# Optimization experiments

Measured on AMD Instinct MI355X. Metric: run time of the kernel, lower is better.

Reference implementation:

```python
import jax, jax.numpy as jnp
from jax import lax
import numpy as np

B, DIM, L_IN = 8, 512, 4096
SCALE = 2
KSIZE = 17
DN = ('NCH', 'OIH', 'NCH')  # conv1d dimension numbers


def _aa_kernel(kernel_size: int, scale: int) -> np.ndarray:
    # replicates scipy.signal.kaiser_atten / kaiser_beta / windows.kaiser
    atten = 2.285 * (kernel_size - 1) * np.pi * (1.0 / scale) + 7.95
    if atten > 50:
        beta = 0.1102 * (atten - 8.7)
    elif atten > 21:
        beta = 0.5842 * (atten - 21) ** 0.4 + 0.07886 * (atten - 21)
    else:
        beta = 0.0
    win = np.kaiser(kernel_size, beta)
    xk = np.arange(kernel_size) - kernel_size // 2
    k = np.sinc(xk / scale) * win  # normalized sinc, same as torch.sinc
    return (k / k.sum()).astype(np.float32)


def setup_inputs() -> dict:
    key = jax.random.key(0)
    k1, k2, k3, k4, k5 = jax.random.split(key, 5)
    kconv = 2 * SCALE - 1
    return {
        'x': jax.random.normal(k1, (B, DIM, L_IN), dtype=jnp.float32),
        'conv_w': jax.random.normal(k2, (DIM, DIM, kconv), dtype=jnp.float32) * (1.0 / np.sqrt(DIM * kconv)),
        'conv_b': jax.random.normal(k3, (DIM,), dtype=jnp.float32) * 0.01,
        'aa_kernel': jnp.asarray(_aa_kernel(KSIZE, SCALE)),
        'proj_w': jax.random.normal(k4, (DIM, DIM), dtype=jnp.float32) * (1.0 / np.sqrt(DIM)),
        'proj_b': jax.random.normal(k5, (DIM,), dtype=jnp.float32) * 0.01,
    }


def reference(x, conv_w, conv_b, aa_kernel, proj_w, proj_b):
    s = SCALE
    # zero-insertion upsample + Conv1d(dim,dim,2s-1,pad=s-1) fused via lhs_dilation.
    # Torch zero-inserts to length l*s (trailing s-1 zeros), so right pad is 2s-2.
    y = lax.conv_general_dilated(
        x, conv_w, window_strides=(1,), padding=[(s - 1, 2 * s - 2)],
        lhs_dilation=(s,), dimension_numbers=DN,
    ) + conv_b[None, :, None]  # [B, D, l*s]
    # depthwise anti-alias filter (same Kaiser-sinc kernel per channel)
    dw = jnp.broadcast_to(aa_kernel, (DIM, 1, KSIZE))
    y = lax.conv_general_dilated(
        y, dw, window_strides=(1,), padding=[(KSIZE // 2, KSIZE // 2)],
        feature_group_count=DIM, dimension_numbers=DN,
    )
    # pointwise 1x1 projection
    return jnp.einsum('bdl,ed->bel', y, proj_w) + proj_b[None, :, None]
```

## Files before the change

kernel.cpp:

```cpp
#include <hip/hip_runtime.h>
#include <hip/hip_bf16.h>

#define BB_   8
#define DIM_  512
#define LIN_  4096
#define LOUT_ 8192

typedef __attribute__((ext_vector_type(8))) __bf16 bf16x8;
typedef __attribute__((ext_vector_type(4))) float  f32x4;
typedef __attribute__((ext_vector_type(8))) unsigned short u16x8;

__device__ __forceinline__ float bf2f(unsigned short u) {
  union { unsigned int i; float f; } x;
  x.i = ((unsigned int)u) << 16;
  return x.f;
}

__device__ __forceinline__ unsigned short f2bf(float f) {
  unsigned int u = __float_as_uint(f);
  return (unsigned short)((u + 0x7fffu + ((u >> 16) & 1u)) >> 16);
}

__device__ __forceinline__ void gload16(const void* g, void* l) {
  __builtin_amdgcn_global_load_lds(
      (__attribute__((address_space(1))) void*)(g),
      (__attribute__((address_space(3))) void*)(l), 16, 0, 0);
}

__global__ __launch_bounds__(256) void k_prep(const float* __restrict__ proj_w,
                                              const float* __restrict__ conv_w,
                                              const float* __restrict__ conv_b,
                                              const float* __restrict__ x,
                                              unsigned short* __restrict__ Mst,
                                              float* __restrict__ Pcb,
                                              unsigned short* __restrict__ Xbt) {
  __shared__ __align__(16) float sm[4160];
  const int bx  = blockIdx.x;
  const int tid = threadIdx.x;

  if (bx < 192) {
    float* Pt = sm;
    float* Wt = sm + 1088;
    const int kk = bx >> 6;
    const int t6 = bx & 63;
    const int et = (t6 >> 3) << 6;
    const int it = (t6 & 7) << 6;
    const int tx = tid & 15, ty = tid >> 4;
    const int le = tid & 63, lg = tid >> 6;
    float acc[4][4] = {};
    for (int d0 = 0; d0 < DIM_; d0 += 16) {
      {
        const float4 v = *(const float4*)&proj_w[(size_t)(et + le) * DIM_ + d0 + lg * 4];
        Pt[(lg * 4 + 0) * 68 + le] = v.x;
        Pt[(lg * 4 + 1) * 68 + le] = v.y;
        Pt[(lg * 4 + 2) * 68 + le] = v.z;
        Pt[(lg * 4 + 3) * 68 + le] = v.w;
      }
#pragma unroll
      for (int r = 0; r < 4; ++r) {
        const int dl = r * 4 + lg;
        Wt[dl * 68 + le] = conv_w[(size_t)(d0 + dl) * (DIM_ * 3) + (it + le) * 3 + kk];
      }
      __syncthreads();
#pragma unroll
      for (int dl = 0; dl < 16; ++dl) {
        const float4 pv = *(const float4*)&Pt[dl * 68 + ty * 4];
        const float4 wv = *(const float4*)&Wt[dl * 68 + tx * 4];
        const float pa[4] = {pv.x, pv.y, pv.z, pv.w};
        const float wa[4] = {wv.x, wv.y, wv.z, wv.w};
#pragma unroll
        for (int a = 0; a < 4; ++a)
#pragma unroll
          for (int b = 0; b < 4; ++b) acc[a][b] += pa[a] * wa[b];
      }
      __syncthreads();
    }
#pragma unroll
    for (int a = 0; a < 4; ++a) {
      uint2 pk;
      pk.x = (unsigned int)f2bf(acc[a][0]) | ((unsigned int)f2bf(acc[a][1]) << 16);
      pk.y = (unsigned int)f2bf(acc[a][2]) | ((unsigned int)f2bf(acc[a][3]) << 16);
      *(uint2*)&Mst[(size_t)(kk * DIM_ + et + ty * 4 + a) * DIM_ + it + tx * 4] = pk;
    }
  } else if (bx < 320) {
    const int idx = bx - 192;
    const int e = idx * 4 + (tid >> 6);
    const int j = tid & 63;
    float s = 0.f;
#pragma unroll
    for (int d = j; d < DIM_; d += 64) s += proj_w[(size_t)e * DIM_ + d] * conv_b[d];
#pragma unroll
    for (int off = 32; off > 0; off >>= 1) s += __shfl_down(s, off, 64);
    if (j == 0) Pcb[e] = s;
  } else {
    const int bc = bx - 320;
    const int bb = bc >> 9;
    const int dt = ((bc >> 6) & 7) << 6;
    const int lt = (bc & 63) << 6;
    const int lr  = tid >> 4;
    const int lc4 = (tid & 15) << 2;
#pragma unroll
    for (int r = 0; r < 4; ++r) {
      const int d = r * 16 + lr;
      const float4 v = *(const float4*)&x[((size_t)(bb * DIM_ + dt + d) << 12) + lt + lc4];
      float* row = sm + d * 65 + lc4;
      row[0] = v.x; row[1] = v.y; row[2] = v.z; row[3] = v.w;
    }
    __syncthreads();
#pragma unroll
    for (int rr = 0; rr < 2; ++rr) {
      const int flat = rr * 256 + tid;
      const int l  = flat >> 3;
      const int d8 = (flat & 7) << 3;
      unsigned int w[4];
#pragma unroll
      for (int p = 0; p < 4; ++p) {
        const float f0 = sm[(d8 + 2 * p + 0) * 65 + l];
        const float f1 = sm[(d8 + 2 * p + 1) * 65 + l];
        w[p] = (unsigned int)f2bf(f0) | ((unsigned int)f2bf(f1) << 16);
      }
      uint4 pk; pk.x = w[0]; pk.y = w[1]; pk.z = w[2]; pk.w = w[3];
      *(uint4*)&Xbt[((size_t)(bb * LIN_ + lt + l) << 9) + dt + d8] = pk;
    }
  }
}

__global__ __launch_bounds__(512, 1) void k_fused(const unsigned short* __restrict__ Xbt,
                                                  const unsigned short* __restrict__ Mst,
                                                  const float* __restrict__ Pcb,
                                                  const float* __restrict__ aa,
                                                  const float* __restrict__ proj_b,
                                                  float* __restrict__ out) {
  __shared__ __align__(16) char lds[131072];
  const int tid = threadIdx.x;
  const int bid = blockIdx.x;
  const int wgs   = (bid & 7) * 128 + (bid >> 3);
  const int ntile = wgs >> 3;
  const int etile = wgs & 7;
  const int bb = ntile >> 4;
  const int L0 = (ntile & 15) << 8;
  const int l0g = L0 - 16;
  const int e0 = etile << 6;

  const int wave = tid >> 6;
  const int lane = tid & 63;

  const unsigned short* src[4];
  int ldso[4];
  {
    const int rl = lane >> 2;
    const int sl = lane & 3;
    const int ch = sl ^ ((rl >> 1) & 3);
#pragma unroll
    for (int i = 0; i < 4; ++i) {
      const int u  = wave + 8 * i;
      const int uu = (u >= 30) ? (u - 30) : u;
      const unsigned short* p;
      if (uu < 12) {
        const int kk = uu >> 2;
        const int er = e0 + ((uu & 3) << 4) + rl;
        p = Mst + ((size_t)(kk * 512 + er) << 9);
      } else {
        int labs = l0g + (uu - 12) * 16 + rl;
        labs = labs < 0 ? 0 : (labs > 4095 ? 4095 : labs);
        p = Xbt + ((size_t)(bb * LIN_ + labs) << 9);
      }
      src[i] = p + (ch << 3);
      ldso[i] = u << 10;
    }
  }

#define STAGE_(kt_, buf_)                              \
  do {                                                 \
    char* base_ = lds + (buf_) * 32768;                \
    gload16(src[0] + (kt_) * 32, base_ + ldso[0]);     \
    gload16(src[1] + (kt_) * 32, base_ + ldso[1]);     \
    gload16(src[2] + (kt_) * 32, base_ + ldso[2]);     \
    gload16(src[3] + (kt_) * 32, base_ + ldso[3]);     \
  } while (0)

  const int wm = wave >> 1;
  const int wn = wave & 1;
  const int lrow = lane & 15;
  const int lc   = lane >> 4;
  const int asl  = lc ^ ((lrow >> 1) & 3);
  const char* A0 = lds + ((wm * 48 + lrow) * 64 + asl * 16);
  const char* B0 = lds + (12288 + (wn * 144 + lrow) * 64 + asl * 16);

  f32x4 acc[3][9] = {};
  bf16x8 afr[2][3], bfr[2][9];

  STAGE_(0, 0); STAGE_(1, 1);
  asm volatile("s_waitcnt vmcnt(4)" ::: "memory");
  __builtin_amdgcn_s_barrier();
  __builtin_amdgcn_sched_barrier(0);
#pragma unroll
  for (int mt = 0; mt < 3; ++mt) afr[0][mt] = *(const bf16x8*)(A0 + mt * 1024);
#pragma unroll
  for (int nt = 0; nt < 9; ++nt) bfr[0][nt] = *(const bf16x8*)(B0 + nt * 1024);

#pragma unroll
  for (int kt = 0; kt < 16; ++kt) {
    const int cur = kt & 1, nxt = cur ^ 1;
    if (kt < 14) {
      STAGE_(kt + 2, (kt + 2) & 3);
      asm volatile("s_waitcnt vmcnt(4)" ::: "memory");
    } else {
      asm volatile("s_waitcnt vmcnt(0)" ::: "memory");
    }
    __builtin_amdgcn_s_barrier();
    __builtin_amdgcn_sched_barrier(0);

    if (kt < 15) {
      const int bo = ((kt + 1) & 3) * 32768;
#pragma unroll
      for (int mt = 0; mt < 3; ++mt)
        afr[nxt][mt] = *(const bf16x8*)(A0 + bo + mt * 1024);
#pragma unroll
      for (int nt = 0; nt < 9; ++nt)
        bfr[nxt][nt] = *(const bf16x8*)(B0 + bo + nt * 1024);
    }

    __builtin_amdgcn_s_setprio(1);
#pragma unroll
    for (int mt = 0; mt < 3; ++mt)
#pragma unroll
      for (int nt = 0; nt < 9; ++nt)
        acc[mt][nt] = __builtin_amdgcn_mfma_f32_16x16x32_bf16(bfr[cur][nt],
                                                              afr[cur][mt],
                                                              acc[mt][nt], 0, 0, 0);
    __builtin_amdgcn_s_setprio(0);
  }
#undef STAGE_
  __builtin_amdgcn_s_barrier();

  unsigned short* Ut = (unsigned short*)lds;
#pragma unroll
  for (int mt = 0; mt < 3; ++mt) {
    const int m = wm * 48 + mt * 16 + lrow;
#pragma unroll
    for (int nt = 0; nt < 9; ++nt) {
      const int lcol = wn * 144 + nt * 16 + (lc << 2);
      uint2 pk;
      pk.x = (unsigned int)f2bf(acc[mt][nt][0]) | ((unsigned int)f2bf(acc[mt][nt][1]) << 16);
      pk.y = (unsigned int)f2bf(acc[mt][nt][2]) | ((unsigned int)f2bf(acc[mt][nt][3]) << 16);
      *(uint2*)&Ut[m * 296 + lcol] = pk;
    }
  }
  __syncthreads();

  const int el  = tid >> 3;
  const int lt0 = (tid & 7) << 5;
  const int e   = e0 + el;
  const float pcb = Pcb[e];
  const float pb  = proj_b[e];
  float sa[17];
#pragma unroll
  for (int j = 0; j < 17; ++j) sa[j] = aa[j];
  const unsigned short* u0r = Ut + (size_t)el * 296;
  const unsigned short* u1r = Ut + (size_t)(64 + el) * 296;
  const unsigned short* u2r = Ut + (size_t)(128 + el) * 296;
  const bool edge = (L0 == 0) || (L0 == 3840);
  float* orow = out + (((size_t)(bb * 512 + e)) << 13) + 2 * (size_t)(L0 + lt0);

#pragma unroll
  for (int cc = 0; cc < 4; ++cc) {
    const int c0 = lt0 + 8 * cc + 12;
    float E[17], O[16];
    if (!edge) {
      const u16x8 e0v = *(const u16x8*)(u1r + c0 - 4);
      const u16x8 e1v = *(const u16x8*)(u1r + c0 + 4);
      const u16x8 e2v = *(const u16x8*)(u1r + c0 + 12);
      const u16x8 a0v = *(const u16x8*)(u0r + c0 - 4);
      const u16x8 a1v = *(const u16x8*)(u0r + c0 + 4);
      const u16x8 a2v = *(const u16x8*)(u0r + c0 + 12);
      const u16x8 b0v = *(const u16x8*)(u2r + c0 - 4);
      const u16x8 b1v = *(const u16x8*)(u2r + c0 + 4);
      const u16x8 b2v = *(const u16x8*)(u2r + c0 + 12);
      unsigned short ue[24], ua[24], ub[24];
#pragma unroll
      for (int j = 0; j < 8; ++j) {
        ue[j] = e0v[j]; ue[j + 8] = e1v[j]; ue[j + 16] = e2v[j];
        ua[j] = a0v[j]; ua[j + 8] = a1v[j]; ua[j + 16] = a2v[j];
        ub[j] = b0v[j]; ub[j + 8] = b1v[j]; ub[j + 16] = b2v[j];
      }
#pragma unroll
      for (int j = 0; j < 17; ++j) E[j] = bf2f(ue[4 + j]) + pcb;
#pragma unroll
      for (int j = 0; j < 16; ++j) O[j] = bf2f(ua[4 + j]) + pcb + bf2f(ub[5 + j]);
    } else {
      const int lt = L0 + lt0 + 8 * cc;
#pragma unroll
      for (int j = 0; j < 17; ++j) {
        const int l = lt - 4 + j;
        E[j] = (l >= 0 && l < 4096) ? (bf2f(u1r[c0 + j]) + pcb) : 0.f;
      }
#pragma unroll
      for (int j = 0; j < 16; ++j) {
        const int l = lt - 4 + j;
        float v = 0.f;
        if (l >= 0 && l < 4096) {
          v = bf2f(u0r[c0 + j]) + pcb;
          if (l + 1 < 4096) v += bf2f(u2r[c0 + j + 1]);
        }
        O[j] = v;
      }
    }
    float res[16];
#pragma unroll
    for (int t = 0; t < 8; ++t) {
      float se = 0.f, so = 0.f;
#pragma unroll
      for (int q = 0; q <= 8; ++q) {
        se += sa[2 * q] * E[t + q];
        so += sa[2 * q] * O[t + q];
      }
#pragma unroll
      for (int q = 0; q < 8; ++q) {
        se += sa[2 * q + 1] * O[t + q];
        so += sa[2 * q + 1] * E[t + q + 1];
      }
      res[2 * t]     = se + pb;
      res[2 * t + 1] = so + pb;
    }
#pragma unroll
    for (int c2 = 0; c2 < 4; ++c2)
      *(float4*)(orow + 16 * cc + 4 * c2) = *(const float4*)&res[4 * c2];
  }
}

extern "C" void kernel_launch(void* const* d_in, const int* in_sizes, int n_in,
                              void* d_out, int out_size, void* d_ws, size_t ws_size,
                              hipStream_t stream) {
  const float* x      = (const float*)d_in[0];
  const float* conv_w = (const float*)d_in[1];
  const float* conv_b = (const float*)d_in[2];
  const float* aa     = (const float*)d_in[3];
  const float* proj_w = (const float*)d_in[4];
  const float* proj_b = (const float*)d_in[5];
  float* out = (float*)d_out;

  char* ws = (char*)d_ws;
  unsigned short* Mst = (unsigned short*)ws;
  float*          Pcb = (float*)(ws + 1572864);
  unsigned short* Xbt = (unsigned short*)(ws + 1574912);

  k_prep<<<dim3(4416, 1, 1), 256, 0, stream>>>(proj_w, conv_w, conv_b, x, Mst, Pcb, Xbt);
  k_fused<<<dim3(1024, 1, 1), 512, 0, stream>>>(Xbt, Mst, Pcb, aa, proj_b, out);
}
```

Before: 322.0 us.

## Split GEMM main loop into two interleaved phases with staged global loads

Restructures the MFMA main loop from register double-buffered fragments into two half-phases per k-step. Each phase loads part of the B fragments from LDS, issues half of the global-to-LDS prefetches, synchronizes, then runs its MFMA subset. The aim is to cut register pressure and interleave memory issue with compute, in the style of ping-pong scheduling. It adds three barriers per iteration, exposes LDS read latency with lgkmcnt(0) waits before the MFMAs, and changes the vmcnt accounting, which risks stalls or correctness issues.

```diff
diff --git a/kernel.cpp b/kernel.cpp
--- a/kernel.cpp
+++ b/kernel.cpp
@@ -170,11 +170,15 @@
     }
   }
 
-#define STAGE_(kt_, buf_)                              \
+#define STAGE2A_(kt_, buf_)                            \
   do {                                                 \
     char* base_ = lds + (buf_) * 32768;                \
     gload16(src[0] + (kt_) * 32, base_ + ldso[0]);     \
     gload16(src[1] + (kt_) * 32, base_ + ldso[1]);     \
+  } while (0)
+#define STAGE2B_(kt_, buf_)                            \
+  do {                                                 \
+    char* base_ = lds + (buf_) * 32768;                \
     gload16(src[2] + (kt_) * 32, base_ + ldso[2]);     \
     gload16(src[3] + (kt_) * 32, base_ + ldso[3]);     \
   } while (0)
@@ -188,51 +192,58 @@
   const char* B0 = lds + (12288 + (wn * 144 + lrow) * 64 + asl * 16);
 
   f32x4 acc[3][9] = {};
-  bf16x8 afr[2][3], bfr[2][9];
-
-  STAGE_(0, 0); STAGE_(1, 1);
+
+  STAGE2A_(0, 0); STAGE2B_(0, 0);
+  STAGE2A_(1, 1); STAGE2B_(1, 1);
   asm volatile("s_waitcnt vmcnt(4)" ::: "memory");
   __builtin_amdgcn_s_barrier();
-  __builtin_amdgcn_sched_barrier(0);
-#pragma unroll
-  for (int mt = 0; mt < 3; ++mt) afr[0][mt] = *(const bf16x8*)(A0 + mt * 1024);
-#pragma unroll
-  for (int nt = 0; nt < 9; ++nt) bfr[0][nt] = *(const bf16x8*)(B0 + nt * 1024);
 
 #pragma unroll
   for (int kt = 0; kt < 16; ++kt) {
-    const int cur = kt & 1, nxt = cur ^ 1;
-    if (kt < 14) {
-      STAGE_(kt + 2, (kt + 2) & 3);
-      asm volatile("s_waitcnt vmcnt(4)" ::: "memory");
-    } else {
-      asm volatile("s_waitcnt vmcnt(0)" ::: "memory");
-    }
+    const int bo = (kt & 3) * 32768;
+    bf16x8 af[3], bfv[9];
+
+#pragma unroll
+    for (int mt = 0; mt < 3; ++mt) af[mt] = *(const bf16x8*)(A0 + bo + mt * 1024);
+#pragma unroll
+    for (int nt = 0; nt < 4; ++nt) bfv[nt] = *(const bf16x8*)(B0 + bo + nt * 1024);
+    if (kt < 14) STAGE2A_(kt + 2, (kt + 2) & 3);
     __builtin_amdgcn_s_barrier();
+    asm volatile("s_waitcnt lgkmcnt(0)" ::: "memory");
     __builtin_amdgcn_sched_barrier(0);
-
-    if (kt < 15) {
-      const int bo = ((kt + 1) & 3) * 32768;
-#pragma unroll
-      for (int mt = 0; mt < 3; ++mt)
-        afr[nxt][mt] = *(const bf16x8*)(A0 + bo + mt * 1024);
-#pragma unroll
-      for (int nt = 0; nt < 9; ++nt)
-        bfr[nxt][nt] = *(const bf16x8*)(B0 + bo + nt * 1024);
-    }
-
     __builtin_amdgcn_s_setprio(1);
 #pragma unroll
     for (int mt = 0; mt < 3; ++mt)
 #pragma unroll
-      for (int nt = 0; nt < 9; ++nt)
-        acc[mt][nt] = __builtin_amdgcn_mfma_f32_16x16x32_bf16(bfr[cur][nt],
-                                                              afr[cur][mt],
+      for (int nt = 0; nt < 4; ++nt)
+        acc[mt][nt] = __builtin_amdgcn_mfma_f32_16x16x32_bf16(bfv[nt], af[mt],
                                                               acc[mt][nt], 0, 0, 0);
     __builtin_amdgcn_s_setprio(0);
-  }
-#undef STAGE_
-  __builtin_amdgcn_s_barrier();
+
+#pragma unroll
+    for (int nt = 4; nt < 9; ++nt) bfv[nt] = *(const bf16x8*)(B0 + bo + nt * 1024);
+    if (kt < 14) STAGE2B_(kt + 2, (kt + 2) & 3);
+    __builtin_amdgcn_s_barrier();
+    asm volatile("s_waitcnt lgkmcnt(0)" ::: "memory");
+    __builtin_amdgcn_sched_barrier(0);
+    __builtin_amdgcn_s_setprio(1);
+#pragma unroll
+    for (int mt = 0; mt < 3; ++mt)
+#pragma unroll
+      for (int nt = 4; nt < 9; ++nt)
+        acc[mt][nt] = __builtin_amdgcn_mfma_f32_16x16x32_bf16(bfv[nt], af[mt],
+                                                              acc[mt][nt], 0, 0, 0);
+    __builtin_amdgcn_s_setprio(0);
+
+    if (kt < 14) {
+      asm volatile("s_waitcnt vmcnt(4)" ::: "memory");
+    } else if (kt == 14) {
+      asm volatile("s_waitcnt vmcnt(0)" ::: "memory");
+    }
+    __builtin_amdgcn_s_barrier();
+  }
+#undef STAGE2A_
+#undef STAGE2B_
 
   unsigned short* Ut = (unsigned short*)lds;
 #pragma unroll
```

New measurement: 317.6 us. No clear change (-1.4%).
